# Optimization experiments

Hardware: AMD Instinct MI355X
Metric: run time of the kernel (lower is better)

## Reference

```python
import jax, jax.numpy as jnp
import numpy as np

N = 170000      # nodes (ogbn-arxiv scale)
E = 2720000     # edges (avg degree 16)
IN, H, L, OUT = 128, 256, 4, 40
BN_EPS = 1e-5


def setup_inputs() -> dict:
    key = jax.random.key(0)
    ks = jax.random.split(key, 6)
    x = jax.random.normal(ks[0], (N, IN), jnp.float32)
    edge_index = jax.random.randint(ks[1], (2, E), 0, N, dtype=jnp.int64)
    W_in = jax.random.normal(ks[2], (IN, H), jnp.float32) * 0.05
    b_in = jnp.zeros((H,), jnp.float32)
    W_hid = jax.random.normal(ks[3], (L - 1, H, H), jnp.float32) * 0.05
    b_hid = jnp.zeros((L - 1, H), jnp.float32)
    gamma = jnp.ones((L, H), jnp.float32)
    beta = jnp.zeros((L, H), jnp.float32)
    W_out = jax.random.normal(ks[4], (L * H, OUT), jnp.float32) * 0.05
    b_out = jnp.zeros((OUT,), jnp.float32)
    return dict(x=x, edge_index=edge_index, W_in=W_in, b_in=b_in,
                W_hid=W_hid, b_hid=b_hid, gamma=gamma, beta=beta,
                W_out=W_out, b_out=b_out)


def _gcn_aggregate(h, src, dst, norm_e, inv_deg):
    # message passing with symmetric normalization + self-loop term
    msg = h[src] * norm_e[:, None]                      # [E, H] gather
    agg = jax.ops.segment_sum(msg, dst, num_segments=N)  # [N, H] scatter-add
    return agg + h * inv_deg[:, None]                   # self-loop: deg^-1


def reference(x, edge_index, W_in, b_in, W_hid, b_hid, gamma, beta, W_out, b_out):
    src, dst = edge_index[0], edge_index[1]
    # degree (incl. self-loop), PyG gcn_norm style
    deg = jax.ops.segment_sum(jnp.ones((E,), x.dtype), dst, num_segments=N) + 1.0
    dinv = jax.lax.rsqrt(deg)
    norm_e = dinv[src] * dinv[dst]
    inv_deg = 1.0 / deg

    outs = []
    h = x
    for i in range(L):
        W = W_in if i == 0 else W_hid[i - 1]
        b = b_in if i == 0 else b_hid[i - 1]
        h = _gcn_aggregate(h @ W, src, dst, norm_e, inv_deg) + b
        # BatchNorm1d (training-mode batch statistics, biased variance)
        mean = jnp.mean(h, axis=0)
        var = jnp.mean(jnp.square(h - mean), axis=0)
        h = (h - mean) * jax.lax.rsqrt(var + BN_EPS) * gamma[i] + beta[i]
        h = jax.nn.relu(h)  # dropout is identity in eval mode
        outs.append(h)

    z = jnp.concatenate(outs, axis=-1) @ W_out + b_out  # JK 'cat' -> [N, L*H] @ [L*H, OUT]
    return jax.nn.log_softmax(z, axis=-1)
```

## Files before the change

kernel.cpp:

```cpp
#include <hip/hip_runtime.h>
#include <math.h>

constexpr int kN = 170000;
constexpr int kE = 2720000;
constexpr int kFin = 128;
constexpr int kFh = 256;
constexpr int kL = 4;
constexpr int kFout = 40;

typedef __attribute__((ext_vector_type(8))) short bf16x8;
typedef __attribute__((ext_vector_type(4))) float f32x4;

__device__ __forceinline__ float jk_b2f(unsigned short u) {
    unsigned int x = ((unsigned int)u) << 16;
    float f;
    __builtin_memcpy(&f, &x, 4);
    return f;
}
__device__ __forceinline__ unsigned short jk_f2b(float f) {
    unsigned int x;
    __builtin_memcpy(&x, &f, 4);
    unsigned int r = (x + 0x7fffu + ((x >> 16) & 1u)) >> 16;
    return (unsigned short)r;
}

union U4 {
    uint4 v;
    unsigned short s[8];
};
union U2 {
    uint2 v;
    unsigned short s[4];
};

__global__ void jka_zero_i(int* p, int n) {
    int i = blockIdx.x * blockDim.x + threadIdx.x;
    if (i < n) p[i] = 0;
}
__global__ void jka_zero_f(float* p, int n) {
    int i = blockIdx.x * blockDim.x + threadIdx.x;
    if (i < n) p[i] = 0.0f;
}

__global__ void jka_detect(const int* eb, int* flag) {
    __shared__ int nz;
    if (threadIdx.x == 0) nz = 0;
    __syncthreads();
    int bad = 0;
    for (int j = 0; j < 4; j++) {
        int idx = threadIdx.x * 4 + j;
        if (eb[2 * idx + 1] != 0) bad = 1;
    }
    if (bad) atomicOr(&nz, 1);
    __syncthreads();
    if (threadIdx.x == 0) {
        flag[0] = nz ? 0 : 1;
        flag[1] = 0;
    }
}

__global__ void jka_count(const int* eb, const int* flag, int* counts, int* rank) {
    int e0 = (blockIdx.x * blockDim.x + threadIdx.x) * 4;
    if (e0 >= kE) return;
    int s64 = flag[0];
    int d[4];
    if (s64) {
        int4 c1 = *(const int4*)(eb + 2 * ((size_t)kE + e0));
        int4 c2 = *(const int4*)(eb + 2 * ((size_t)kE + e0) + 4);
        d[0] = c1.x; d[1] = c1.z; d[2] = c2.x; d[3] = c2.z;
    } else {
        int4 c1 = *(const int4*)(eb + (size_t)kE + e0);
        d[0] = c1.x; d[1] = c1.y; d[2] = c1.z; d[3] = c1.w;
    }
    int r[4];
#pragma unroll
    for (int q = 0; q < 4; q++) r[q] = atomicAdd(&counts[d[q]], 1);
    *(int4*)(rank + e0) = make_int4(r[0], r[1], r[2], r[3]);
}

__global__ void jka_nodeprep(const int* counts, float* dinv, float* invdeg, int* off,
                             int* cursor) {
    int n = blockIdx.x * blockDim.x + threadIdx.x;
    if (n < kN) {
        int c = counts[n];
        float deg = (float)c + 1.0f;
        dinv[n] = rsqrtf(deg);
        invdeg[n] = 1.0f / deg;
        off[n] = atomicAdd(cursor, c);
    }
}

__global__ void jka_fill(const int* eb, const int* flag, const int* rank, const int* off,
                         const float* dinv, int2* csr) {
    int e0 = (blockIdx.x * blockDim.x + threadIdx.x) * 4;
    if (e0 >= kE) return;
    int s64 = flag[0];
    int s[4], d[4];
    if (s64) {
        int4 a1 = *(const int4*)(eb + 2 * (size_t)e0);
        int4 a2 = *(const int4*)(eb + 2 * (size_t)e0 + 4);
        s[0] = a1.x; s[1] = a1.z; s[2] = a2.x; s[3] = a2.z;
        int4 c1 = *(const int4*)(eb + 2 * ((size_t)kE + e0));
        int4 c2 = *(const int4*)(eb + 2 * ((size_t)kE + e0) + 4);
        d[0] = c1.x; d[1] = c1.z; d[2] = c2.x; d[3] = c2.z;
    } else {
        int4 a1 = *(const int4*)(eb + (size_t)e0);
        s[0] = a1.x; s[1] = a1.y; s[2] = a1.z; s[3] = a1.w;
        int4 c1 = *(const int4*)(eb + (size_t)kE + e0);
        d[0] = c1.x; d[1] = c1.y; d[2] = c1.z; d[3] = c1.w;
    }
    int4 rr = *(const int4*)(rank + e0);
    int r[4] = {rr.x, rr.y, rr.z, rr.w};
#pragma unroll
    for (int q = 0; q < 4; q++) {
        int p = off[d[q]] + r[q];
        float w = dinv[s[q]] * dinv[d[q]];
        csr[p] = make_int2(s[q], __float_as_int(w));
    }
}

__global__ void jka_prepw(const float* W_in, const float* W_hid, const float* Wout,
                          unsigned short* Wt0, unsigned short* Wt1, unsigned short* Wto) {
    int idx = blockIdx.x * blockDim.x + threadIdx.x;
    if (idx < 32768) {
        int c = idx >> 7, k = idx & 127;
        Wt0[idx] = jk_f2b(W_in[(size_t)k * kFh + c]);
    } else if (idx < 32768 + 196608) {
        int t2 = idx - 32768;
        int l = t2 >> 16, rem = t2 & 65535;
        int c = rem >> 8, k = rem & 255;
        Wt1[(size_t)l * 65536 + rem] = jk_f2b(W_hid[(size_t)l * 65536 + k * kFh + c]);
    } else if (idx < 32768 + 196608 + 49152) {
        int t2 = idx - 32768 - 196608;
        int l = t2 / (48 * 256), rem = t2 % (48 * 256);
        int col = rem >> 8, k = rem & 255;
        float wv = (col < kFout) ? Wout[(size_t)(l * kFh + k) * kFout + col] : 0.f;
        unsigned short hi = jk_f2b(wv);
        unsigned short lo = jk_f2b(wv - jk_b2f(hi));
        Wto[((size_t)(l * 2 + 0) * 48 + col) * 256 + k] = hi;
        Wto[((size_t)(l * 2 + 1) * 48 + col) * 256 + k] = lo;
    }
}

__global__ void jka_xb(const float* x, unsigned short* xb) {
    int i = blockIdx.x * blockDim.x + threadIdx.x;
    if (i >= kN * kFin / 8) return;
    float4 a = *(const float4*)(x + (size_t)i * 8);
    float4 b = *(const float4*)(x + (size_t)i * 8 + 4);
    U4 o;
    o.s[0] = jk_f2b(a.x); o.s[1] = jk_f2b(a.y); o.s[2] = jk_f2b(a.z); o.s[3] = jk_f2b(a.w);
    o.s[4] = jk_f2b(b.x); o.s[5] = jk_f2b(b.y); o.s[6] = jk_f2b(b.z); o.s[7] = jk_f2b(b.w);
    *(uint4*)(xb + (size_t)i * 8) = o.v;
}

template <int MODE>
__global__ __launch_bounds__(256) void jka_gemm(const unsigned short* A, const unsigned short* Wt,
                                                unsigned short* C, int K, const float* sc,
                                                const float* sh, const float* bias,
                                                float* stats) {
    __shared__ unsigned short As[128][40];
    __shared__ unsigned short Bs[128][40];
    __shared__ float ssc[256], ssh[256];
    __shared__ float csum[128], csq[128];
    int tid = threadIdx.x;
    if (MODE == 1) {
        ssc[tid] = sc[tid];
        ssh[tid] = sh[tid];
    } else {
        ssc[tid] = bias[tid];
        if (tid < 128) { csum[tid] = 0.f; csq[tid] = 0.f; }
    }
    __syncthreads();
    int row0 = blockIdx.x * 128;
    int n0 = blockIdx.y * 128;
    int lane = tid & 63, w = tid >> 6;
    int wm = w >> 1, wn = w & 1;
    int lr = lane & 15, lg = lane >> 4;

    f32x4 acc[4][4];
#pragma unroll
    for (int i = 0; i < 4; i++)
#pragma unroll
        for (int j = 0; j < 4; j++) acc[i][j] = (f32x4){0.f, 0.f, 0.f, 0.f};

    int sr = tid >> 1;
    int skh = (tid & 1) * 16;

    for (int k0 = 0; k0 < K; k0 += 32) {
        {
            int row = row0 + sr;
            if (MODE == 0) {
                uint4 u0 = make_uint4(0, 0, 0, 0), u1 = make_uint4(0, 0, 0, 0);
                if (row < kN) {
                    const unsigned short* g = A + (size_t)row * K + k0 + skh;
                    u0 = *(const uint4*)g;
                    u1 = *(const uint4*)(g + 8);
                }
                *(uint4*)&As[sr][skh] = u0;
                *(uint4*)&As[sr][skh + 8] = u1;
            } else {
                U4 o0, o1;
                if (row < kN) {
                    U4 u0, u1;
                    const unsigned short* g = A + (size_t)row * K + k0 + skh;
                    u0.v = *(const uint4*)g;
                    u1.v = *(const uint4*)(g + 8);
#pragma unroll
                    for (int j = 0; j < 8; j++) {
                        float v = jk_b2f(u0.s[j]) * ssc[k0 + skh + j] + ssh[k0 + skh + j];
                        o0.s[j] = jk_f2b(v > 0.f ? v : 0.f);
                    }
#pragma unroll
                    for (int j = 0; j < 8; j++) {
                        float v = jk_b2f(u1.s[j]) * ssc[k0 + skh + 8 + j] + ssh[k0 + skh + 8 + j];
                        o1.s[j] = jk_f2b(v > 0.f ? v : 0.f);
                    }
                } else {
#pragma unroll
                    for (int j = 0; j < 8; j++) { o0.s[j] = 0; o1.s[j] = 0; }
                }
                *(uint4*)&As[sr][skh] = o0.v;
                *(uint4*)&As[sr][skh + 8] = o1.v;
            }
        }
        {
            const unsigned short* g = Wt + (size_t)(n0 + sr) * K + k0 + skh;
            *(uint4*)&Bs[sr][skh] = *(const uint4*)g;
            *(uint4*)&Bs[sr][skh + 8] = *(const uint4*)(g + 8);
        }
        __syncthreads();

        bf16x8 af[4], bfr[4];
#pragma unroll
        for (int mi = 0; mi < 4; mi++)
            af[mi] = *(const bf16x8*)&As[wm * 64 + mi * 16 + lr][lg * 8];
#pragma unroll
        for (int ni = 0; ni < 4; ni++)
            bfr[ni] = *(const bf16x8*)&Bs[wn * 64 + ni * 16 + lr][lg * 8];
#pragma unroll
        for (int mi = 0; mi < 4; mi++)
#pragma unroll
            for (int ni = 0; ni < 4; ni++)
                acc[mi][ni] = __builtin_amdgcn_mfma_f32_16x16x32_bf16(af[mi], bfr[ni],
                                                                      acc[mi][ni], 0, 0, 0);
        __syncthreads();
    }

    float ps[4] = {0.f, 0.f, 0.f, 0.f}, pq[4] = {0.f, 0.f, 0.f, 0.f};
#pragma unroll
    for (int mi = 0; mi < 4; mi++) {
#pragma unroll
        for (int j = 0; j < 4; j++) {
            int row = row0 + wm * 64 + mi * 16 + lg * 4 + j;
            if (row < kN) {
#pragma unroll
                for (int ni = 0; ni < 4; ni++) {
                    int col = n0 + wn * 64 + ni * 16 + lr;
                    float v = acc[mi][ni][j];
                    if (MODE == 0) {
                        v += ssc[col];
                        ps[ni] += v;
                        pq[ni] += v * v;
                    }
                    C[(size_t)row * kFh + col] = jk_f2b(v);
                }
            }
        }
    }
    if (MODE == 0) {
#pragma unroll
        for (int ni = 0; ni < 4; ni++) {
            int lc = wn * 64 + ni * 16 + lr;
            atomicAdd(&csum[lc], ps[ni]);
            atomicAdd(&csq[lc], pq[ni]);
        }
        __syncthreads();
        if (tid < 128) {
            atomicAdd(&stats[n0 + tid], csum[tid]);
            atomicAdd(&stats[256 + n0 + tid], csq[tid]);
        }
    }
}

template <int CH, int HASB>
__global__ __launch_bounds__(256) void jka_agg(const unsigned short* t, const float* bias,
                                               const int* off, const int* cnt, const int2* csr,
                                               const float* invdeg, unsigned short* h) {
    constexpr int PC = CH / 32;
    constexpr int DEPTH = (CH == 128) ? 8 : 4;
    int n = blockIdx.x * 8 + (threadIdx.x >> 5);
    if (n >= kN) return;
    int c0 = (threadIdx.x & 31) * PC;

    float acc[PC];
    {
        float sw = invdeg[n];
        if constexpr (PC == 8) {
            U4 u;
            u.v = *(const uint4*)(t + (size_t)n * CH + c0);
#pragma unroll
            for (int j = 0; j < 8; j++) acc[j] = sw * jk_b2f(u.s[j]);
        } else {
            U2 u;
            u.v = *(const uint2*)(t + (size_t)n * CH + c0);
#pragma unroll
            for (int j = 0; j < 4; j++) acc[j] = sw * jk_b2f(u.s[j]);
        }
    }

    int base = off[n], c = cnt[n];
    for (int i = 0; i < c; i += DEPTH) {
        float w[DEPTH];
        U4 u8[PC == 8 ? DEPTH : 1];
        U2 u4[PC == 4 ? DEPTH : 1];
#pragma unroll
        for (int q = 0; q < DEPTH; q++) {
            int e = i + q;
            bool v = e < c;
            int2 cw = csr[v ? base + e : base];
            w[q] = v ? __int_as_float(cw.y) : 0.0f;
            if constexpr (PC == 8)
                u8[q].v = *(const uint4*)(t + (size_t)cw.x * CH + c0);
            else
                u4[q].v = *(const uint2*)(t + (size_t)cw.x * CH + c0);
        }
#pragma unroll
        for (int q = 0; q < DEPTH; q++) {
            if constexpr (PC == 8) {
#pragma unroll
                for (int j = 0; j < 8; j++) acc[j] += w[q] * jk_b2f(u8[q].s[j]);
            } else {
#pragma unroll
                for (int j = 0; j < 4; j++) acc[j] += w[q] * jk_b2f(u4[q].s[j]);
            }
        }
    }

    if constexpr (PC == 8) {
        U4 o;
#pragma unroll
        for (int j = 0; j < 8; j++)
            o.s[j] = jk_f2b(HASB ? acc[j] + bias[c0 + j] : acc[j]);
        *(uint4*)(h + (size_t)n * CH + c0) = o.v;
    } else {
        U2 o;
#pragma unroll
        for (int j = 0; j < 4; j++)
            o.s[j] = jk_f2b(HASB ? acc[j] + bias[c0 + j] : acc[j]);
        *(uint2*)(h + (size_t)n * CH + c0) = o.v;
    }
}

__global__ __launch_bounds__(256) void jka_bnstats(const unsigned short* h, float* stats) {
    __shared__ float lsum[256], lsq[256];
    int tid = threadIdx.x;
    lsum[tid] = 0.f;
    lsq[tid] = 0.f;
    __syncthreads();
    int c0 = (tid & 31) * 8;
    int grp = tid >> 5;
    float rs[8] = {}, rq[8] = {};
    for (int n = blockIdx.x * 8 + grp; n < kN; n += gridDim.x * 8) {
        U4 u;
        u.v = *(const uint4*)(h + (size_t)n * kFh + c0);
#pragma unroll
        for (int j = 0; j < 8; j++) {
            float v = jk_b2f(u.s[j]);
            rs[j] += v;
            rq[j] += v * v;
        }
    }
#pragma unroll
    for (int j = 0; j < 8; j++) {
        atomicAdd(&lsum[c0 + j], rs[j]);
        atomicAdd(&lsq[c0 + j], rq[j]);
    }
    __syncthreads();
    atomicAdd(&stats[tid], lsum[tid]);
    atomicAdd(&stats[256 + tid], lsq[tid]);
}

__global__ void jka_bnfinal(const float* stats, const float* gamma, const float* beta, int layer,
                            float* scale, float* shift) {
    int c = threadIdx.x;
    float mean = stats[c] / (float)kN;
    float var = stats[256 + c] / (float)kN - mean * mean;
    var = var < 0.f ? 0.f : var;
    float sc = gamma[layer * kFh + c] * rsqrtf(var + 1e-5f);
    scale[c] = sc;
    shift[c] = beta[layer * kFh + c] - mean * sc;
}

template <int FIRST, int LAST>
__global__ __launch_bounds__(256) void jka_zacc(const unsigned short* h, const float* scale,
                                                const float* shift, const unsigned short* Wto,
                                                const float* bout, float* z, float* out) {
    __shared__ unsigned short Bs[2][48][264];
    __shared__ unsigned short As[128][40];
    __shared__ float ssc[256], ssh[256];
    int tid = threadIdx.x;
    for (int f = tid; f < 2 * 48 * 256; f += 256) {
        int hl = f / (48 * 256);
        int rem = f % (48 * 256);
        Bs[hl][rem >> 8][rem & 255] = Wto[f];
    }
    ssc[tid] = scale[tid];
    ssh[tid] = shift[tid];
    __syncthreads();

    int row0 = blockIdx.x * 128;
    int w = tid >> 6, lane = tid & 63;
    int lr = lane & 15, lg = lane >> 4;
    int sr = tid >> 1, skh = (tid & 1) * 16;

    f32x4 acc[2][3];
#pragma unroll
    for (int mi = 0; mi < 2; mi++)
#pragma unroll
        for (int ni = 0; ni < 3; ni++) acc[mi][ni] = (f32x4){0.f, 0.f, 0.f, 0.f};

    for (int k0 = 0; k0 < kFh; k0 += 32) {
        int row = row0 + sr;
        U4 o0, o1;
        if (row < kN) {
            U4 u0, u1;
            const unsigned short* g = h + (size_t)row * kFh + k0 + skh;
            u0.v = *(const uint4*)g;
            u1.v = *(const uint4*)(g + 8);
#pragma unroll
            for (int j = 0; j < 8; j++) {
                float v = jk_b2f(u0.s[j]) * ssc[k0 + skh + j] + ssh[k0 + skh + j];
                o0.s[j] = jk_f2b(v > 0.f ? v : 0.f);
            }
#pragma unroll
            for (int j = 0; j < 8; j++) {
                float v = jk_b2f(u1.s[j]) * ssc[k0 + skh + 8 + j] + ssh[k0 + skh + 8 + j];
                o1.s[j] = jk_f2b(v > 0.f ? v : 0.f);
            }
        } else {
#pragma unroll
            for (int j = 0; j < 8; j++) { o0.s[j] = 0; o1.s[j] = 0; }
        }
        *(uint4*)&As[sr][skh] = o0.v;
        *(uint4*)&As[sr][skh + 8] = o1.v;
        __syncthreads();

        bf16x8 af[2], bh[3], bl[3];
#pragma unroll
        for (int mi = 0; mi < 2; mi++)
            af[mi] = *(const bf16x8*)&As[w * 32 + mi * 16 + lr][lg * 8];
#pragma unroll
        for (int ni = 0; ni < 3; ni++) {
            bh[ni] = *(const bf16x8*)&Bs[0][ni * 16 + lr][k0 + lg * 8];
            bl[ni] = *(const bf16x8*)&Bs[1][ni * 16 + lr][k0 + lg * 8];
        }
#pragma unroll
        for (int mi = 0; mi < 2; mi++)
#pragma unroll
            for (int ni = 0; ni < 3; ni++) {
                acc[mi][ni] = __builtin_amdgcn_mfma_f32_16x16x32_bf16(af[mi], bh[ni],
                                                                      acc[mi][ni], 0, 0, 0);
                acc[mi][ni] = __builtin_amdgcn_mfma_f32_16x16x32_bf16(af[mi], bl[ni],
                                                                      acc[mi][ni], 0, 0, 0);
            }
        __syncthreads();
    }

#pragma unroll
    for (int mi = 0; mi < 2; mi++) {
#pragma unroll
        for (int j = 0; j < 4; j++) {
            int row = row0 + w * 32 + mi * 16 + lg * 4 + j;
            if (row >= kN) continue;
            if (!LAST) {
#pragma unroll
                for (int ni = 0; ni < 3; ni++) {
                    int col = ni * 16 + lr;
                    if (col < kFout) {
                        if (FIRST)
                            z[(size_t)row * kFout + col] = acc[mi][ni][j] + bout[col];
                        else
                            z[(size_t)row * kFout + col] += acc[mi][ni][j];
                    }
                }
            } else {
                const float* zp = z + (size_t)row * kFout;
                float v0 = zp[lr] + acc[mi][0][j];
                float v1 = zp[16 + lr] + acc[mi][1][j];
                float v2 = (lr < 8) ? (zp[32 + lr] + acc[mi][2][j]) : -1e30f;
                float m = fmaxf(fmaxf(v0, v1), v2);
                m = fmaxf(m, __shfl_xor(m, 1, 64));
                m = fmaxf(m, __shfl_xor(m, 2, 64));
                m = fmaxf(m, __shfl_xor(m, 4, 64));
                m = fmaxf(m, __shfl_xor(m, 8, 64));
                float s = expf(v0 - m) + expf(v1 - m) + ((lr < 8) ? expf(v2 - m) : 0.f);
                s += __shfl_xor(s, 1, 64);
                s += __shfl_xor(s, 2, 64);
                s += __shfl_xor(s, 4, 64);
                s += __shfl_xor(s, 8, 64);
                float ls = m + logf(s);
                float* op = out + (size_t)row * kFout;
                op[lr] = v0 - ls;
                op[16 + lr] = v1 - ls;
                if (lr < 8) op[32 + lr] = v2 - ls;
            }
        }
    }
}

extern "C" void kernel_launch(void* const* d_in, const int* in_sizes, int n_in,
                              void* d_out, int out_size, void* d_ws, size_t ws_size,
                              hipStream_t stream) {
    (void)in_sizes; (void)n_in; (void)out_size; (void)ws_size;
    const float* x = (const float*)d_in[0];
    const int* eb = (const int*)d_in[1];
    const float* W_in = (const float*)d_in[2];
    const float* b_in = (const float*)d_in[3];
    const float* W_hid = (const float*)d_in[4];
    const float* b_hid = (const float*)d_in[5];
    const float* gamma = (const float*)d_in[6];
    const float* beta = (const float*)d_in[7];
    const float* W_out = (const float*)d_in[8];
    const float* b_out = (const float*)d_in[9];
    float* out = (float*)d_out;

    char* p = (char*)d_ws;
    auto alloc = [&](size_t b) -> void* {
        void* r = (void*)p;
        p += (b + 255) & ~(size_t)255;
        return r;
    };
    int* flag = (int*)alloc(8);
    int* counts = (int*)alloc((size_t)kN * 4);
    int* off = (int*)alloc((size_t)kN * 4);
    float* dinv = (float*)alloc((size_t)kN * 4);
    float* invdeg = (float*)alloc((size_t)kN * 4);
    float* bnsums = (float*)alloc((size_t)kL * 512 * 4);
    float* bnss = (float*)alloc((size_t)kL * 512 * 4);
    int* rank = (int*)alloc((size_t)kE * 4);
    int2* csr = (int2*)alloc((size_t)kE * 8);
    unsigned short* hA = (unsigned short*)alloc((size_t)kN * kFh * 2);
    unsigned short* hB = (unsigned short*)alloc((size_t)kN * kFh * 2);
    float* z = (float*)alloc((size_t)kN * kFout * 4);
    unsigned short* Wt0 = (unsigned short*)alloc((size_t)kFin * kFh * 2);
    unsigned short* Wt1 = (unsigned short*)alloc((size_t)3 * kFh * kFh * 2);
    unsigned short* Wto = (unsigned short*)alloc((size_t)kL * 2 * 48 * 256 * 2);

    jka_zero_i<<<(kN + 255) / 256, 256, 0, stream>>>(counts, kN);
    jka_zero_f<<<(kL * 512 + 255) / 256, 256, 0, stream>>>(bnsums, kL * 512);
    jka_detect<<<1, 256, 0, stream>>>(eb, flag);
    jka_count<<<(kE / 4 + 255) / 256, 256, 0, stream>>>(eb, flag, counts, rank);
    jka_nodeprep<<<(kN + 255) / 256, 256, 0, stream>>>(counts, dinv, invdeg, off, flag + 1);
    jka_fill<<<(kE / 4 + 255) / 256, 256, 0, stream>>>(eb, flag, rank, off, dinv, csr);
    jka_prepw<<<(32768 + 196608 + 49152 + 255) / 256, 256, 0, stream>>>(W_in, W_hid, W_out,
                                                                        Wt0, Wt1, Wto);
    jka_xb<<<(kN * kFin / 8 + 255) / 256, 256, 0, stream>>>(x, hB);
    jka_agg<128, 0><<<(kN + 7) / 8, 256, 0, stream>>>(hB, nullptr, off, counts, csr, invdeg,
                                                      hA);

    unsigned short* Wts[4] = {Wt0, Wt1, Wt1 + 65536, Wt1 + 131072};
    dim3 gg((kN + 127) / 128, 2);
    int zg = (kN + 127) / 128;
    for (int l = 0; l < kL; l++) {
        float* st = bnsums + (size_t)l * 512;
        if (l == 0) {
            jka_gemm<0><<<gg, 256, 0, stream>>>(hA, Wts[0], hB, kFin, nullptr, nullptr, b_in,
                                                st);
        } else {
            const float* b = b_hid + (size_t)(l - 1) * kFh;
            float* scp = bnss + (size_t)(l - 1) * 512;
            jka_gemm<1><<<gg, 256, 0, stream>>>(hB, Wts[l], hA, kFh, scp, scp + 256, nullptr,
                                                nullptr);
            jka_agg<256, 1><<<(kN + 7) / 8, 256, 0, stream>>>(hA, b, off, counts, csr, invdeg,
                                                              hB);
            jka_bnstats<<<1024, 256, 0, stream>>>(hB, st);
        }
        jka_bnfinal<<<1, 256, 0, stream>>>(st, gamma, beta, l, bnss + (size_t)l * 512,
                                           bnss + (size_t)l * 512 + 256);
        const unsigned short* wtl = Wto + (size_t)l * 2 * 48 * 256;
        float* sc = bnss + (size_t)l * 512;
        if (l == 0)
            jka_zacc<1, 0><<<zg, 256, 0, stream>>>(hB, sc, sc + 256, wtl, b_out, z, out);
        else if (l < kL - 1)
            jka_zacc<0, 0><<<zg, 256, 0, stream>>>(hB, sc, sc + 256, wtl, b_out, z, out);
        else
            jka_zacc<0, 1><<<zg, 256, 0, stream>>>(hB, sc, sc + 256, wtl, b_out, z, out);
    }
}
```

Baseline: 1.648 ms.

## Fuse JK output projection into next layer GEMM and drop hi/lo split

Computes the JK output projection for layers 0-2 inside the next layer's hidden GEMM (only on the blockIdx.y==0 column tiles), reusing the already-normalized A fragments in shared memory. This removes three separate zacc passes over the node features. It also drops the bf16 hi/lo split of W_out, so the projection runs with a single bf16 MFMA instead of two. The cost is lower precision in the output projection and extra load imbalance, since only half the GEMM blocks do the added work and read Wtz straight from global memory.

```diff
diff --git a/kernel.cpp b/kernel.cpp
--- a/kernel.cpp
+++ b/kernel.cpp
@@ -33,16 +33,16 @@
     unsigned short s[4];
 };
 
-__global__ void jka_zero_i(int* p, int n) {
+__global__ void jkb_zero_i(int* p, int n) {
     int i = blockIdx.x * blockDim.x + threadIdx.x;
     if (i < n) p[i] = 0;
 }
-__global__ void jka_zero_f(float* p, int n) {
+__global__ void jkb_zero_f(float* p, int n) {
     int i = blockIdx.x * blockDim.x + threadIdx.x;
     if (i < n) p[i] = 0.0f;
 }
 
-__global__ void jka_detect(const int* eb, int* flag) {
+__global__ void jkb_detect(const int* eb, int* flag) {
     __shared__ int nz;
     if (threadIdx.x == 0) nz = 0;
     __syncthreads();
@@ -59,7 +59,7 @@
     }
 }
 
-__global__ void jka_count(const int* eb, const int* flag, int* counts, int* rank) {
+__global__ void jkb_count(const int* eb, const int* flag, int* counts, int* rank) {
     int e0 = (blockIdx.x * blockDim.x + threadIdx.x) * 4;
     if (e0 >= kE) return;
     int s64 = flag[0];
@@ -78,7 +78,7 @@
     *(int4*)(rank + e0) = make_int4(r[0], r[1], r[2], r[3]);
 }
 
-__global__ void jka_nodeprep(const int* counts, float* dinv, float* invdeg, int* off,
+__global__ void jkb_nodeprep(const int* counts, float* dinv, float* invdeg, int* off,
                              int* cursor) {
     int n = blockIdx.x * blockDim.x + threadIdx.x;
     if (n < kN) {
@@ -90,7 +90,7 @@
     }
 }
 
-__global__ void jka_fill(const int* eb, const int* flag, const int* rank, const int* off,
+__global__ void jkb_fill(const int* eb, const int* flag, const int* rank, const int* off,
                          const float* dinv, int2* csr) {
     int e0 = (blockIdx.x * blockDim.x + threadIdx.x) * 4;
     if (e0 >= kE) return;
@@ -119,7 +119,7 @@
     }
 }
 
-__global__ void jka_prepw(const float* W_in, const float* W_hid, const float* Wout,
+__global__ void jkb_prepw(const float* W_in, const float* W_hid, const float* Wout,
                           unsigned short* Wt0, unsigned short* Wt1, unsigned short* Wto) {
     int idx = blockIdx.x * blockDim.x + threadIdx.x;
     if (idx < 32768) {
@@ -135,14 +135,11 @@
         int l = t2 / (48 * 256), rem = t2 % (48 * 256);
         int col = rem >> 8, k = rem & 255;
         float wv = (col < kFout) ? Wout[(size_t)(l * kFh + k) * kFout + col] : 0.f;
-        unsigned short hi = jk_f2b(wv);
-        unsigned short lo = jk_f2b(wv - jk_b2f(hi));
-        Wto[((size_t)(l * 2 + 0) * 48 + col) * 256 + k] = hi;
-        Wto[((size_t)(l * 2 + 1) * 48 + col) * 256 + k] = lo;
-    }
-}
-
-__global__ void jka_xb(const float* x, unsigned short* xb) {
+        Wto[(size_t)t2] = jk_f2b(wv);
+    }
+}
+
+__global__ void jkb_xb(const float* x, unsigned short* xb) {
     int i = blockIdx.x * blockDim.x + threadIdx.x;
     if (i >= kN * kFin / 8) return;
     float4 a = *(const float4*)(x + (size_t)i * 8);
@@ -153,11 +150,12 @@
     *(uint4*)(xb + (size_t)i * 8) = o.v;
 }
 
-template <int MODE>
-__global__ __launch_bounds__(256) void jka_gemm(const unsigned short* A, const unsigned short* Wt,
+template <int MODE, int FIRSTZ>
+__global__ __launch_bounds__(256) void jkb_gemm(const unsigned short* A, const unsigned short* Wt,
                                                 unsigned short* C, int K, const float* sc,
                                                 const float* sh, const float* bias,
-                                                float* stats) {
+                                                float* stats, const unsigned short* Wtz,
+                                                const float* bout, float* z) {
     __shared__ unsigned short As[128][40];
     __shared__ unsigned short Bs[128][40];
     __shared__ float ssc[256], ssh[256];
@@ -176,12 +174,18 @@
     int lane = tid & 63, w = tid >> 6;
     int wm = w >> 1, wn = w & 1;
     int lr = lane & 15, lg = lane >> 4;
+    bool doz = (MODE == 1) && (blockIdx.y == 0);
 
     f32x4 acc[4][4];
 #pragma unroll
     for (int i = 0; i < 4; i++)
 #pragma unroll
         for (int j = 0; j < 4; j++) acc[i][j] = (f32x4){0.f, 0.f, 0.f, 0.f};
+    f32x4 accz[2][3];
+#pragma unroll
+    for (int i = 0; i < 2; i++)
+#pragma unroll
+        for (int j = 0; j < 3; j++) accz[i][j] = (f32x4){0.f, 0.f, 0.f, 0.f};
 
     int sr = tid >> 1;
     int skh = (tid & 1) * 16;
@@ -243,6 +247,19 @@
             for (int ni = 0; ni < 4; ni++)
                 acc[mi][ni] = __builtin_amdgcn_mfma_f32_16x16x32_bf16(af[mi], bfr[ni],
                                                                       acc[mi][ni], 0, 0, 0);
+        if (doz) {
+            bf16x8 bz[3];
+#pragma unroll
+            for (int ni = 0; ni < 3; ni++)
+                bz[ni] = *(const bf16x8*)(Wtz + ((size_t)(ni * 16 + lr) << 8) + k0 + lg * 8);
+#pragma unroll
+            for (int mzi = 0; mzi < 2; mzi++) {
+#pragma unroll
+                for (int ni = 0; ni < 3; ni++)
+                    accz[mzi][ni] = __builtin_amdgcn_mfma_f32_16x16x32_bf16(
+                        af[wn * 2 + mzi], bz[ni], accz[mzi][ni], 0, 0, 0);
+            }
+        }
         __syncthreads();
     }
 
@@ -280,10 +297,30 @@
             atomicAdd(&stats[256 + n0 + tid], csq[tid]);
         }
     }
+    if (doz) {
+#pragma unroll
+        for (int mzi = 0; mzi < 2; mzi++) {
+#pragma unroll
+            for (int j = 0; j < 4; j++) {
+                int row = row0 + wm * 64 + (wn * 2 + mzi) * 16 + lg * 4 + j;
+                if (row >= kN) continue;
+#pragma unroll
+                for (int ni = 0; ni < 3; ni++) {
+                    int col = ni * 16 + lr;
+                    if (col < kFout) {
+                        if (FIRSTZ)
+                            z[(size_t)row * kFout + col] = accz[mzi][ni][j] + bout[col];
+                        else
+                            z[(size_t)row * kFout + col] += accz[mzi][ni][j];
+                    }
+                }
+            }
+        }
+    }
 }
 
 template <int CH, int HASB>
-__global__ __launch_bounds__(256) void jka_agg(const unsigned short* t, const float* bias,
+__global__ __launch_bounds__(256) void jkb_agg(const unsigned short* t, const float* bias,
                                                const int* off, const int* cnt, const int2* csr,
                                                const float* invdeg, unsigned short* h) {
     constexpr int PC = CH / 32;
@@ -351,7 +388,7 @@
     }
 }
 
-__global__ __launch_bounds__(256) void jka_bnstats(const unsigned short* h, float* stats) {
+__global__ __launch_bounds__(256) void jkb_bnstats(const unsigned short* h, float* stats) {
     __shared__ float lsum[256], lsq[256];
     int tid = threadIdx.x;
     lsum[tid] = 0.f;
@@ -380,7 +417,7 @@
     atomicAdd(&stats[256 + tid], lsq[tid]);
 }
 
-__global__ void jka_bnfinal(const float* stats, const float* gamma, const float* beta, int layer,
+__global__ void jkb_bnfinal(const float* stats, const float* gamma, const float* beta, int layer,
                             float* scale, float* shift) {
     int c = threadIdx.x;
     float mean = stats[c] / (float)kN;
@@ -391,18 +428,15 @@
     shift[c] = beta[layer * kFh + c] - mean * sc;
 }
 
-template <int FIRST, int LAST>
-__global__ __launch_bounds__(256) void jka_zacc(const unsigned short* h, const float* scale,
-                                                const float* shift, const unsigned short* Wto,
-                                                const float* bout, float* z, float* out) {
-    __shared__ unsigned short Bs[2][48][264];
+__global__ __launch_bounds__(256) void jkb_zlast(const unsigned short* h, const float* scale,
+                                                 const float* shift, const unsigned short* Wto,
+                                                 float* z, float* out) {
+    __shared__ unsigned short Bs[48][264];
     __shared__ unsigned short As[128][40];
     __shared__ float ssc[256], ssh[256];
     int tid = threadIdx.x;
-    for (int f = tid; f < 2 * 48 * 256; f += 256) {
-        int hl = f / (48 * 256);
-        int rem = f % (48 * 256);
-        Bs[hl][rem >> 8][rem & 255] = Wto[f];
+    for (int f = tid; f < 48 * 256; f += 256) {
+        Bs[f >> 8][f & 255] = Wto[f];
     }
     ssc[tid] = scale[tid];
     ssh[tid] = shift[tid];
@@ -445,24 +479,19 @@
         *(uint4*)&As[sr][skh + 8] = o1.v;
         __syncthreads();
 
-        bf16x8 af[2], bh[3], bl[3];
+        bf16x8 af[2], bh[3];
 #pragma unroll
         for (int mi = 0; mi < 2; mi++)
             af[mi] = *(const bf16x8*)&As[w * 32 + mi * 16 + lr][lg * 8];
 #pragma unroll
-        for (int ni = 0; ni < 3; ni++) {
-            bh[ni] = *(const bf16x8*)&Bs[0][ni * 16 + lr][k0 + lg * 8];
-            bl[ni] = *(const bf16x8*)&Bs[1][ni * 16 + lr][k0 + lg * 8];
-        }
+        for (int ni = 0; ni < 3; ni++)
+            bh[ni] = *(const bf16x8*)&Bs[ni * 16 + lr][k0 + lg * 8];
 #pragma unroll
         for (int mi = 0; mi < 2; mi++)
 #pragma unroll
-            for (int ni = 0; ni < 3; ni++) {
+            for (int ni = 0; ni < 3; ni++)
                 acc[mi][ni] = __builtin_amdgcn_mfma_f32_16x16x32_bf16(af[mi], bh[ni],
                                                                       acc[mi][ni], 0, 0, 0);
-                acc[mi][ni] = __builtin_amdgcn_mfma_f32_16x16x32_bf16(af[mi], bl[ni],
-                                                                      acc[mi][ni], 0, 0, 0);
-            }
         __syncthreads();
     }
 
@@ -472,38 +501,25 @@
         for (int j = 0; j < 4; j++) {
             int row = row0 + w * 32 + mi * 16 + lg * 4 + j;
             if (row >= kN) continue;
-            if (!LAST) {
-#pragma unroll
-                for (int ni = 0; ni < 3; ni++) {
-                    int col = ni * 16 + lr;
-                    if (col < kFout) {
-                        if (FIRST)
-                            z[(size_t)row * kFout + col] = acc[mi][ni][j] + bout[col];
-                        else
-                            z[(size_t)row * kFout + col] += acc[mi][ni][j];
-                    }
-                }
-            } else {
-                const float* zp = z + (size_t)row * kFout;
-                float v0 = zp[lr] + acc[mi][0][j];
-                float v1 = zp[16 + lr] + acc[mi][1][j];
-                float v2 = (lr < 8) ? (zp[32 + lr] + acc[mi][2][j]) : -1e30f;
-                float m = fmaxf(fmaxf(v0, v1), v2);
-                m = fmaxf(m, __shfl_xor(m, 1, 64));
-                m = fmaxf(m, __shfl_xor(m, 2, 64));
-                m = fmaxf(m, __shfl_xor(m, 4, 64));
-                m = fmaxf(m, __shfl_xor(m, 8, 64));
-                float s = expf(v0 - m) + expf(v1 - m) + ((lr < 8) ? expf(v2 - m) : 0.f);
-                s += __shfl_xor(s, 1, 64);
-                s += __shfl_xor(s, 2, 64);
-                s += __shfl_xor(s, 4, 64);
-                s += __shfl_xor(s, 8, 64);
-                float ls = m + logf(s);
-                float* op = out + (size_t)row * kFout;
-                op[lr] = v0 - ls;
-                op[16 + lr] = v1 - ls;
-                if (lr < 8) op[32 + lr] = v2 - ls;
-            }
+            const float* zp = z + (size_t)row * kFout;
+            float v0 = zp[lr] + acc[mi][0][j];
+            float v1 = zp[16 + lr] + acc[mi][1][j];
+            float v2 = (lr < 8) ? (zp[32 + lr] + acc[mi][2][j]) : -1e30f;
+            float m = fmaxf(fmaxf(v0, v1), v2);
+            m = fmaxf(m, __shfl_xor(m, 1, 64));
+            m = fmaxf(m, __shfl_xor(m, 2, 64));
+            m = fmaxf(m, __shfl_xor(m, 4, 64));
+            m = fmaxf(m, __shfl_xor(m, 8, 64));
+            float s = expf(v0 - m) + expf(v1 - m) + ((lr < 8) ? expf(v2 - m) : 0.f);
+            s += __shfl_xor(s, 1, 64);
+            s += __shfl_xor(s, 2, 64);
+            s += __shfl_xor(s, 4, 64);
+            s += __shfl_xor(s, 8, 64);
+            float ls = m + logf(s);
+            float* op = out + (size_t)row * kFout;
+            op[lr] = v0 - ls;
+            op[16 + lr] = v1 - ls;
+            if (lr < 8) op[32 + lr] = v2 - ls;
         }
     }
 }
@@ -544,18 +560,18 @@
     float* z = (float*)alloc((size_t)kN * kFout * 4);
     unsigned short* Wt0 = (unsigned short*)alloc((size_t)kFin * kFh * 2);
     unsigned short* Wt1 = (unsigned short*)alloc((size_t)3 * kFh * kFh * 2);
-    unsigned short* Wto = (unsigned short*)alloc((size_t)kL * 2 * 48 * 256 * 2);
-
-    jka_zero_i<<<(kN + 255) / 256, 256, 0, stream>>>(counts, kN);
-    jka_zero_f<<<(kL * 512 + 255) / 256, 256, 0, stream>>>(bnsums, kL * 512);
-    jka_detect<<<1, 256, 0, stream>>>(eb, flag);
-    jka_count<<<(kE / 4 + 255) / 256, 256, 0, stream>>>(eb, flag, counts, rank);
-    jka_nodeprep<<<(kN + 255) / 256, 256, 0, stream>>>(counts, dinv, invdeg, off, flag + 1);
-    jka_fill<<<(kE / 4 + 255) / 256, 256, 0, stream>>>(eb, flag, rank, off, dinv, csr);
-    jka_prepw<<<(32768 + 196608 + 49152 + 255) / 256, 256, 0, stream>>>(W_in, W_hid, W_out,
+    unsigned short* Wto = (unsigned short*)alloc((size_t)kL * 48 * 256 * 2);
+
+    jkb_zero_i<<<(kN + 255) / 256, 256, 0, stream>>>(counts, kN);
+    jkb_zero_f<<<(kL * 512 + 255) / 256, 256, 0, stream>>>(bnsums, kL * 512);
+    jkb_detect<<<1, 256, 0, stream>>>(eb, flag);
+    jkb_count<<<(kE / 4 + 255) / 256, 256, 0, stream>>>(eb, flag, counts, rank);
+    jkb_nodeprep<<<(kN + 255) / 256, 256, 0, stream>>>(counts, dinv, invdeg, off, flag + 1);
+    jkb_fill<<<(kE / 4 + 255) / 256, 256, 0, stream>>>(eb, flag, rank, off, dinv, csr);
+    jkb_prepw<<<(32768 + 196608 + 49152 + 255) / 256, 256, 0, stream>>>(W_in, W_hid, W_out,
                                                                         Wt0, Wt1, Wto);
-    jka_xb<<<(kN * kFin / 8 + 255) / 256, 256, 0, stream>>>(x, hB);
-    jka_agg<128, 0><<<(kN + 7) / 8, 256, 0, stream>>>(hB, nullptr, off, counts, csr, invdeg,
+    jkb_xb<<<(kN * kFin / 8 + 255) / 256, 256, 0, stream>>>(x, hB);
+    jkb_agg<128, 0><<<(kN + 7) / 8, 256, 0, stream>>>(hB, nullptr, off, counts, csr, invdeg,
                                                       hA);
 
     unsigned short* Wts[4] = {Wt0, Wt1, Wt1 + 65536, Wt1 + 131072};
@@ -564,26 +580,25 @@
     for (int l = 0; l < kL; l++) {
         float* st = bnsums + (size_t)l * 512;
         if (l == 0) {
-            jka_gemm<0><<<gg, 256, 0, stream>>>(hA, Wts[0], hB, kFin, nullptr, nullptr, b_in,
-                                                st);
+            jkb_gemm<0, 0><<<gg, 256, 0, stream>>>(hA, Wts[0], hB, kFin, nullptr, nullptr,
+                                                   b_in, st, nullptr, nullptr, nullptr);
         } else {
             const float* b = b_hid + (size_t)(l - 1) * kFh;
             float* scp = bnss + (size_t)(l - 1) * 512;
-            jka_gemm<1><<<gg, 256, 0, stream>>>(hB, Wts[l], hA, kFh, scp, scp + 256, nullptr,
-                                                nullptr);
-            jka_agg<256, 1><<<(kN + 7) / 8, 256, 0, stream>>>(hA, b, off, counts, csr, invdeg,
+            const unsigned short* wtz = Wto + (size_t)(l - 1) * 48 * 256;
+            if (l == 1)
+                jkb_gemm<1, 1><<<gg, 256, 0, stream>>>(hB, Wts[l], hA, kFh, scp, scp + 256,
+                                                       nullptr, nullptr, wtz, b_out, z);
+            else
+                jkb_gemm<1, 0><<<gg, 256, 0, stream>>>(hB, Wts[l], hA, kFh, scp, scp + 256,
+                                                       nullptr, nullptr, wtz, b_out, z);
+            jkb_agg<256, 1><<<(kN + 7) / 8, 256, 0, stream>>>(hA, b, off, counts, csr, invdeg,
                                                               hB);
-            jka_bnstats<<<1024, 256, 0, stream>>>(hB, st);
-        }
-        jka_bnfinal<<<1, 256, 0, stream>>>(st, gamma, beta, l, bnss + (size_t)l * 512,
+            jkb_bnstats<<<1024, 256, 0, stream>>>(hB, st);
+        }
+        jkb_bnfinal<<<1, 256, 0, stream>>>(st, gamma, beta, l, bnss + (size_t)l * 512,
                                            bnss + (size_t)l * 512 + 256);
-        const unsigned short* wtl = Wto + (size_t)l * 2 * 48 * 256;
-        float* sc = bnss + (size_t)l * 512;
-        if (l == 0)
-            jka_zacc<1, 0><<<zg, 256, 0, stream>>>(hB, sc, sc + 256, wtl, b_out, z, out);
-        else if (l < kL - 1)
-            jka_zacc<0, 0><<<zg, 256, 0, stream>>>(hB, sc, sc + 256, wtl, b_out, z, out);
-        else
-            jka_zacc<0, 1><<<zg, 256, 0, stream>>>(hB, sc, sc + 256, wtl, b_out, z, out);
-    }
-}
+    }
+    jkb_zlast<<<zg, 256, 0, stream>>>(hB, bnss + 3 * 512, bnss + 3 * 512 + 256,
+                                      Wto + (size_t)3 * 48 * 256, z, out);
+}
```

After: 1.765 ms. 7.1% more time.
